# Kernel tuning notes

Hardware: AMD Instinct MI355X
Metric: run time of the kernel (lower is better)

Reference implementation:

```python
import jax, jax.numpy as jnp
import numpy as np

ALPHA = 0.05
KSIZE = 7
SIGMA = 7.0  # SecondMomentMatrixLayer calls get_gaussian_kernel(ksize, ksize)


def _gaussian_kernel(ksize, sigma):
    ax = np.arange(ksize, dtype=np.float32) - (ksize - 1) / 2.0
    g1 = np.exp(-(ax ** 2) / (2.0 * sigma ** 2))
    g2 = np.outer(g1, g1)
    g2 = g2 / g2.sum()
    return jnp.asarray(g2, dtype=jnp.float32)


def setup_inputs() -> dict:
    key = jax.random.key(0)
    x = jax.random.uniform(key, (1, 1, 2048, 4096), dtype=jnp.float32)
    # Sobel filters (cross-correlation weights, as torch conv2d uses)
    wx = jnp.array([[-1., 0., 1.], [-2., 0., 2.], [-1., 0., 1.]], dtype=jnp.float32)
    wy = wx.T
    sobel_w = jnp.stack([wx, wy], axis=0)[:, None]  # (2,1,3,3)
    gauss_w = _gaussian_kernel(KSIZE, SIGMA)[None, None]  # (1,1,7,7)
    return {"x": x, "sobel_w": sobel_w, "gauss_w": gauss_w}


def _conv_same(x, w, groups=1):
    # x: (N,C,H,W), w: (O,C/g,kh,kw); torch-style cross-correlation, SAME padding
    return jax.lax.conv_general_dilated(
        x, w, window_strides=(1, 1), padding="SAME",
        dimension_numbers=("NCHW", "OIHW", "NCHW"),
        feature_group_count=groups)


def reference(x, sobel_w, gauss_w):
    # 1) image gradients: (N,1,H,W) -> (N,2,H,W)
    g = _conv_same(x, sobel_w)
    ix, iy = g[:, 0], g[:, 1]  # (N,H,W)
    # 2) channel products Ixx, Iyy, Ixy: (N,3,H,W)
    prod = jnp.stack([ix * ix, iy * iy, ix * iy], axis=1)
    # 3) Gaussian smoothing of each channel (same kernel depthwise)
    gw3 = jnp.broadcast_to(gauss_w, (3, 1, KSIZE, KSIZE))
    s = _conv_same(prod, gw3, groups=3)
    sxx, syy, sxy = s[:, 0], s[:, 1], s[:, 2]  # (N,H,W)
    # 4) corner response R = det - alpha*trace^2 (with the original's extra unsqueeze(0))
    r = (sxx * syy - sxy * sxy) - ALPHA * ((sxx + syy) ** 2)[None]  # (1,N,H,W) -> (1,1,H,W) for N=1
    # 5) NMS: threshold at (lower) median, 7x7 stride-1 maxpool, equality mask, multiply
    flat = r.ravel()
    k = (flat.shape[0] - 1) // 2  # torch.median -> lower median
    med = jnp.partition(flat, k)[k]
    thr = jnp.where(r > med, r, jnp.float32(0))
    pooled = jax.lax.reduce_window(
        thr, -jnp.inf, jax.lax.max, (1, 1, KSIZE, KSIZE), (1, 1, 1, 1), "SAME")
    mask = jnp.where(pooled == thr, jnp.float32(1), jnp.float32(0))
    return mask * r
```

## Files before the change

### kernel.cpp

```cpp
#include <hip/hip_runtime.h>
#include <hip/hip_bf16.h>
#include <math.h>

#define H 2048
#define W 4096
#define NPIX (H * W)
#define KSEL 4194303u
#define NT 512
#define TSX 64
#define TSY 32
#define NBX (W / TSX)
#define NBY (H / TSY)

__device__ __forceinline__ unsigned fmap(float f) {
    unsigned u = __float_as_uint(f);
    return (u & 0x80000000u) ? ~u : (u | 0x80000000u);
}
__device__ __forceinline__ float4 ld4s(const float* p) { return *(const float4*)p; }
__device__ __forceinline__ void st4s(float* p, float4 v) { *(float4*)p = v; }

#define SMF 13480
#define SXA(r,c) smem[5472 + (r)*76 + (c)]
#define GXA(r,c) smem[(r)*72 + (c)]
#define GYA(r,c) smem[2736 + (r)*72 + (c)]
#define H0A(r,c) smem[5472 + (r)*68 + (c)]
#define H1A(r,c) smem[8056 + (r)*68 + (c)]
#define H2A(r,c) smem[10640 + (r)*68 + (c)]

__global__ __launch_bounds__(NT) void k_response(const float* __restrict__ x,
                                                 const float* __restrict__ gw,
                                                 float* __restrict__ r,
                                                 unsigned* __restrict__ hist1) {
    __shared__ float smem[SMF];
    unsigned* lh = (unsigned*)&smem[13224];

    int tl = threadIdx.x;
    int bx = blockIdx.x & (NBX - 1);
    int by = blockIdx.x >> 6;
    int tx0 = bx * TSX, ty0 = by * TSY;

    float hwr[7], vwr[7];
    float g33 = gw[24];
#pragma unroll
    for (int b = 0; b < 7; ++b) hwr[b] = gw[21 + b];
#pragma unroll
    for (int a = 0; a < 7; ++a) vwr[a] = gw[a * 7 + 3] / g33;

    if (tl < 256) lh[tl] = 0;

#pragma unroll
    for (int it = 0; it < 2; ++it) {
        int task = tl + it * NT;
        if (task < 720) {
            int row = task / 18, g = task - row * 18;
            int gy = ty0 - 4 + row;
            int gx0 = tx0 - 4 + 4 * g;
            float4 v = make_float4(0.f, 0.f, 0.f, 0.f);
            if ((unsigned)gy < H) {
                if ((unsigned)gx0 <= (unsigned)(W - 4)) {
                    v = *(const float4*)&x[(size_t)gy * W + gx0];
                } else {
                    float* vv = (float*)&v;
#pragma unroll
                    for (int k = 0; k < 4; ++k) {
                        int c = gx0 + k;
                        if ((unsigned)c < W) vv[k] = x[(size_t)gy * W + c];
                    }
                }
            }
            st4s(&SXA(row, 4 * g), v);
        }
    }
    __syncthreads();

#pragma unroll
    for (int it = 0; it < 2; ++it) {
        int task = tl + it * NT;
        if (task < 684) {
            int row = task / 18, g = task - row * 18;
            int base = 4 * g;
            float w0[8], w1[8], w2[8];
            {
                float4 t0 = ld4s(&SXA(row, base)), t1 = ld4s(&SXA(row, base + 4));
                w0[0]=t0.x; w0[1]=t0.y; w0[2]=t0.z; w0[3]=t0.w; w0[4]=t1.x; w0[5]=t1.y; w0[6]=t1.z; w0[7]=t1.w;
                t0 = ld4s(&SXA(row + 1, base)); t1 = ld4s(&SXA(row + 1, base + 4));
                w1[0]=t0.x; w1[1]=t0.y; w1[2]=t0.z; w1[3]=t0.w; w1[4]=t1.x; w1[5]=t1.y; w1[6]=t1.z; w1[7]=t1.w;
                t0 = ld4s(&SXA(row + 2, base)); t1 = ld4s(&SXA(row + 2, base + 4));
                w2[0]=t0.x; w2[1]=t0.y; w2[2]=t0.z; w2[3]=t0.w; w2[4]=t1.x; w2[5]=t1.y; w2[6]=t1.z; w2[7]=t1.w;
            }
            int rowOK = ((unsigned)(ty0 - 3 + row) < H);
            float4 gxv, gyv;
            float* pgx = (float*)&gxv;
            float* pgy = (float*)&gyv;
#pragma unroll
            for (int k = 0; k < 4; ++k) {
                float ixv = (w0[k + 2] - w0[k]) + 2.f * (w1[k + 2] - w1[k]) + (w2[k + 2] - w2[k]);
                float iyv = (w2[k] - w0[k]) + 2.f * (w2[k + 1] - w0[k + 1]) + (w2[k + 2] - w0[k + 2]);
                int gc = tx0 + base + k - 3;
                bool ok = rowOK && ((unsigned)gc < W);
                pgx[k] = ok ? ixv : 0.f;
                pgy[k] = ok ? iyv : 0.f;
            }
            st4s(&GXA(row, base), gxv);
            st4s(&GYA(row, base), gyv);
        }
    }
    __syncthreads();

#pragma unroll
    for (int it = 0; it < 2; ++it) {
        int task = tl + it * NT;
        if (task < 608) {
            int row = task >> 4, c0 = (task & 15) * 4;
            float wgx[12], wgy[12];
            {
                float4 t0 = ld4s(&GXA(row, c0)), t1 = ld4s(&GXA(row, c0 + 4)), t2 = ld4s(&GXA(row, c0 + 8));
                wgx[0]=t0.x; wgx[1]=t0.y; wgx[2]=t0.z; wgx[3]=t0.w; wgx[4]=t1.x; wgx[5]=t1.y; wgx[6]=t1.z; wgx[7]=t1.w;
                wgx[8]=t2.x; wgx[9]=t2.y; wgx[10]=t2.z; wgx[11]=t2.w;
                t0 = ld4s(&GYA(row, c0)); t1 = ld4s(&GYA(row, c0 + 4)); t2 = ld4s(&GYA(row, c0 + 8));
                wgy[0]=t0.x; wgy[1]=t0.y; wgy[2]=t0.z; wgy[3]=t0.w; wgy[4]=t1.x; wgy[5]=t1.y; wgy[6]=t1.z; wgy[7]=t1.w;
                wgy[8]=t2.x; wgy[9]=t2.y; wgy[10]=t2.z; wgy[11]=t2.w;
            }
            float px[10], py[10], pxy[10];
#pragma unroll
            for (int i = 0; i < 10; ++i) {
                px[i] = wgx[i] * wgx[i];
                py[i] = wgy[i] * wgy[i];
                pxy[i] = wgx[i] * wgy[i];
            }
            float4 s0, s1, s2;
            float* q0 = (float*)&s0; float* q1 = (float*)&s1; float* q2 = (float*)&s2;
#pragma unroll
            for (int k = 0; k < 4; ++k) {
                float a0 = 0.f, a1 = 0.f, a2 = 0.f;
#pragma unroll
                for (int b = 0; b < 7; ++b) {
                    float w = hwr[b];
                    a0 += w * px[k + b];
                    a1 += w * py[k + b];
                    a2 += w * pxy[k + b];
                }
                q0[k] = a0; q1[k] = a1; q2[k] = a2;
            }
            st4s(&H0A(row, c0), s0);
            st4s(&H1A(row, c0), s1);
            st4s(&H2A(row, c0), s2);
        }
    }
    __syncthreads();

    {
        int ii = tl >> 4, c0 = (tl & 15) * 4;
        float4 a0 = make_float4(0.f, 0.f, 0.f, 0.f), a1 = a0, a2 = a0;
#pragma unroll
        for (int a = 0; a < 7; ++a) {
            float w = vwr[a];
            float4 h0v = ld4s(&H0A(ii + a, c0));
            float4 h1v = ld4s(&H1A(ii + a, c0));
            float4 h2v = ld4s(&H2A(ii + a, c0));
            a0.x += w * h0v.x; a0.y += w * h0v.y; a0.z += w * h0v.z; a0.w += w * h0v.w;
            a1.x += w * h1v.x; a1.y += w * h1v.y; a1.z += w * h1v.z; a1.w += w * h1v.w;
            a2.x += w * h2v.x; a2.y += w * h2v.y; a2.z += w * h2v.z; a2.w += w * h2v.w;
        }
        float* sxx = (float*)&a0; float* syy = (float*)&a1; float* sxy = (float*)&a2;
        float4 rv4;
        float* prv = (float*)&rv4;
#pragma unroll
        for (int k = 0; k < 4; ++k) {
            float tr = sxx[k] + syy[k];
            float rv = sxx[k] * syy[k] - sxy[k] * sxy[k] - 0.05f * tr * tr;
            prv[k] = rv;
        }
        st4s(&r[(size_t)(ty0 + ii) * W + tx0 + c0], rv4);
#pragma unroll
        for (int k = 0; k < 4; ++k) atomicAdd(&lh[fmap(prv[k]) >> 24], 1u);
    }
    __syncthreads();
    if (tl < 256 && lh[tl]) atomicAdd(&hist1[tl], lh[tl]);
}

__global__ __launch_bounds__(256) void k_scan256(const unsigned* __restrict__ hist,
                                                 unsigned* __restrict__ sel,
                                                 int in_rank_idx, int out_base) {
    __shared__ unsigned s[256];
    int t = threadIdx.x;
    unsigned c = hist[t];
    s[t] = c;
    __syncthreads();
    for (int off = 1; off < 256; off <<= 1) {
        unsigned v = (t >= off) ? s[t - off] : 0u;
        __syncthreads();
        s[t] += v;
        __syncthreads();
    }
    unsigned k = (in_rank_idx < 0) ? KSEL : sel[in_rank_idx];
    unsigned cumb = s[t] - c;
    if (k >= cumb && k < s[t]) {
        sel[out_base] = (unsigned)t;
        sel[out_base + 1] = k - cumb;
    }
}

__global__ __launch_bounds__(256) void k_hist2(const float* __restrict__ r,
                                               const unsigned* __restrict__ sel,
                                               unsigned* __restrict__ hist2) {
    __shared__ unsigned lh[256];
    lh[threadIdx.x] = 0;
    __syncthreads();
    unsigned b1 = sel[0];
    int idx = blockIdx.x * blockDim.x + threadIdx.x;
    int stride = gridDim.x * blockDim.x;
    const float4* r4 = (const float4*)r;
    for (int i = idx; i < NPIX / 4; i += stride) {
        float4 v = r4[i];
        unsigned u;
        u = fmap(v.x); if ((u >> 24) == b1) atomicAdd(&lh[(u >> 16) & 0xFF], 1u);
        u = fmap(v.y); if ((u >> 24) == b1) atomicAdd(&lh[(u >> 16) & 0xFF], 1u);
        u = fmap(v.z); if ((u >> 24) == b1) atomicAdd(&lh[(u >> 16) & 0xFF], 1u);
        u = fmap(v.w); if ((u >> 24) == b1) atomicAdd(&lh[(u >> 16) & 0xFF], 1u);
    }
    __syncthreads();
    if (lh[threadIdx.x]) atomicAdd(&hist2[threadIdx.x], lh[threadIdx.x]);
}

__global__ __launch_bounds__(256) void k_hist3(const float* __restrict__ r,
                                               const unsigned* __restrict__ sel,
                                               unsigned* __restrict__ hist3) {
    unsigned top16 = (sel[0] << 8) | sel[2];
    int idx = blockIdx.x * blockDim.x + threadIdx.x;
    int stride = gridDim.x * blockDim.x;
    const float4* r4 = (const float4*)r;
    for (int i = idx; i < NPIX / 4; i += stride) {
        float4 v = r4[i];
        unsigned u;
        u = fmap(v.x); if ((u >> 16) == top16) atomicAdd(&hist3[u & 0xFFFF], 1u);
        u = fmap(v.y); if ((u >> 16) == top16) atomicAdd(&hist3[u & 0xFFFF], 1u);
        u = fmap(v.z); if ((u >> 16) == top16) atomicAdd(&hist3[u & 0xFFFF], 1u);
        u = fmap(v.w); if ((u >> 16) == top16) atomicAdd(&hist3[u & 0xFFFF], 1u);
    }
}

__global__ __launch_bounds__(256) void k_scan64k(const unsigned* __restrict__ hist3,
                                                 unsigned* __restrict__ sel) {
    __shared__ unsigned s[256];
    int t = threadIdx.x;
    unsigned sum = 0;
    for (int i = 0; i < 256; ++i) sum += hist3[t * 256 + i];
    s[t] = sum;
    __syncthreads();
    for (int off = 1; off < 256; off <<= 1) {
        unsigned v = (t >= off) ? s[t - off] : 0u;
        __syncthreads();
        s[t] += v;
        __syncthreads();
    }
    unsigned k = sel[3];
    unsigned cumb = s[t] - sum;
    if (k >= cumb && k < s[t]) {
        unsigned rem = k - cumb;
        unsigned cum = 0, b3 = 0;
        for (int i = 0; i < 256; ++i) {
            unsigned c = hist3[t * 256 + i];
            if (rem < cum + c) { b3 = (unsigned)(t * 256 + i); break; }
            cum += c;
        }
        unsigned med_u = (sel[0] << 24) | (sel[2] << 16) | b3;
        unsigned bits = (med_u & 0x80000000u) ? (med_u & 0x7FFFFFFFu) : ~med_u;
        ((float*)sel)[4] = __uint_as_float(bits);
    }
}

#define RTA(r,c) smem[(r)*76 + (c)]
#define THA(r,c) smem[2888 + (r)*76 + (c)]
#define HMA(r,c) smem[5776 + (r)*68 + (c)]

__global__ __launch_bounds__(NT) void k_final(const float* __restrict__ r,
                                              const unsigned* __restrict__ sel,
                                              float* __restrict__ out) {
    __shared__ float smem[8360];
    float med = ((const float*)sel)[4];
    int tl = threadIdx.x;
    int bx = blockIdx.x & (NBX - 1);
    int by = blockIdx.x >> 6;
    int tx0 = bx * TSX, ty0 = by * TSY;
    const float NINF = -INFINITY;

#pragma unroll
    for (int it = 0; it < 2; ++it) {
        int task = tl + it * NT;
        if (task < 684) {
            int row = task / 18, g = task - row * 18;
            int gy = ty0 - 3 + row;
            int gx0 = tx0 - 4 + 4 * g;
            float4 v = make_float4(NINF, NINF, NINF, NINF);
            float4 tv = v;
            float* pv = (float*)&v; float* ptv = (float*)&tv;
            if ((unsigned)gy < H) {
                if ((unsigned)gx0 <= (unsigned)(W - 4)) {
                    v = *(const float4*)&r[(size_t)gy * W + gx0];
#pragma unroll
                    for (int k = 0; k < 4; ++k) ptv[k] = (pv[k] > med) ? pv[k] : 0.f;
                } else {
#pragma unroll
                    for (int k = 0; k < 4; ++k) {
                        int c = gx0 + k;
                        if ((unsigned)c < W) {
                            float rv = r[(size_t)gy * W + c];
                            pv[k] = rv;
                            ptv[k] = (rv > med) ? rv : 0.f;
                        }
                    }
                }
            }
            st4s(&RTA(row, 4 * g), v);
            st4s(&THA(row, 4 * g), tv);
        }
    }
    __syncthreads();

#pragma unroll
    for (int it = 0; it < 2; ++it) {
        int task = tl + it * NT;
        if (task < 608) {
            int row = task >> 4, c0 = (task & 15) * 4;
            float w[12];
            {
                float4 t0 = ld4s(&THA(row, c0)), t1 = ld4s(&THA(row, c0 + 4)), t2 = ld4s(&THA(row, c0 + 8));
                w[0]=t0.x; w[1]=t0.y; w[2]=t0.z; w[3]=t0.w; w[4]=t1.x; w[5]=t1.y; w[6]=t1.z; w[7]=t1.w;
                w[8]=t2.x; w[9]=t2.y; w[10]=t2.z; w[11]=t2.w;
            }
            float4 m4;
            float* pm = (float*)&m4;
#pragma unroll
            for (int k = 0; k < 4; ++k) {
                float m = w[k + 1];
#pragma unroll
                for (int b = 2; b < 8; ++b) m = fmaxf(m, w[k + b]);
                pm[k] = m;
            }
            st4s(&HMA(row, c0), m4);
        }
    }
    __syncthreads();

    {
        int ii = tl >> 4, c0 = (tl & 15) * 4;
        float4 m = ld4s(&HMA(ii, c0));
#pragma unroll
        for (int a = 1; a < 7; ++a) {
            float4 h = ld4s(&HMA(ii + a, c0));
            m.x = fmaxf(m.x, h.x); m.y = fmaxf(m.y, h.y);
            m.z = fmaxf(m.z, h.z); m.w = fmaxf(m.w, h.w);
        }
        float4 rv = ld4s(&RTA(ii + 3, c0 + 4));
        float4 tv = ld4s(&THA(ii + 3, c0 + 4));
        float4 o;
        o.x = (m.x == tv.x) ? rv.x : 0.f;
        o.y = (m.y == tv.y) ? rv.y : 0.f;
        o.z = (m.z == tv.z) ? rv.z : 0.f;
        o.w = (m.w == tv.w) ? rv.w : 0.f;
        st4s(&out[(size_t)(ty0 + ii) * W + tx0 + c0], o);
    }
}

extern "C" void kernel_launch(void* const* d_in, const int* in_sizes, int n_in,
                              void* d_out, int out_size, void* d_ws, size_t ws_size,
                              hipStream_t stream) {
    const float* x = (const float*)d_in[0];
    const float* gw = (const float*)d_in[2];
    float* out = (float*)d_out;

    char* ws = (char*)d_ws;
    float* r = (float*)ws;
    unsigned* hist1 = (unsigned*)(ws + (size_t)NPIX * 4);
    unsigned* hist2 = hist1 + 256;
    unsigned* hist3 = hist2 + 256;
    unsigned* sel = hist3 + 65536;

    hipMemsetAsync(hist1, 0, (256 + 256 + 65536 + 8) * sizeof(unsigned), stream);

    int nblk = NBX * NBY;
    k_response<<<nblk, NT, 0, stream>>>(x, gw, r, hist1);
    k_scan256<<<1, 256, 0, stream>>>(hist1, sel, -1, 0);
    k_hist2<<<1024, 256, 0, stream>>>(r, sel, hist2);
    k_scan256<<<1, 256, 0, stream>>>(hist2, sel, 1, 2);
    k_hist3<<<1024, 256, 0, stream>>>(r, sel, hist3);
    k_scan64k<<<1, 256, 0, stream>>>(hist3, sel);
    k_final<<<nblk, NT, 0, stream>>>(r, sel, out);
}
```

Measured before the change: 140.7 us.

## Add interior fast paths, widen 64k scan, drop threshold tile from NMS kernel

Interior tiles in the response and final kernels now skip boundary checks on halo loads and Sobel masking. The final-stage median scan runs with 1024 threads using vectorized uint4 loads, which shortens each thread's serial loop. The NMS kernel no longer stores a separate thresholded tile in shared memory; it recomputes the threshold in registers, which cuts shared-memory footprint and stores. The median slot moves from sel[4] to sel[6], which adds an extra branch for -inf padding.

```diff
diff --git a/kernel.cpp b/kernel.cpp
--- a/kernel.cpp
+++ b/kernel.cpp
@@ -18,6 +18,12 @@
 }
 __device__ __forceinline__ float4 ld4s(const float* p) { return *(const float4*)p; }
 __device__ __forceinline__ void st4s(float* p, float4 v) { *(float4*)p = v; }
+__device__ __forceinline__ void ld12(const float* p, float* d) {
+    float4 a = ld4s(p), b = ld4s(p + 4), c = ld4s(p + 8);
+    d[0]=a.x; d[1]=a.y; d[2]=a.z; d[3]=a.w;
+    d[4]=b.x; d[5]=b.y; d[6]=b.z; d[7]=b.w;
+    d[8]=c.x; d[9]=c.y; d[10]=c.z; d[11]=c.w;
+}
 
 #define SMF 13480
 #define SXA(r,c) smem[5472 + (r)*76 + (c)]
@@ -38,6 +44,7 @@
     int bx = blockIdx.x & (NBX - 1);
     int by = blockIdx.x >> 6;
     int tx0 = bx * TSX, ty0 = by * TSY;
+    bool interior = ((unsigned)(bx - 1) < 62u) && ((unsigned)(by - 1) < 62u);
 
     float hwr[7], vwr[7];
     float g33 = gw[24];
@@ -55,16 +62,21 @@
             int row = task / 18, g = task - row * 18;
             int gy = ty0 - 4 + row;
             int gx0 = tx0 - 4 + 4 * g;
-            float4 v = make_float4(0.f, 0.f, 0.f, 0.f);
-            if ((unsigned)gy < H) {
-                if ((unsigned)gx0 <= (unsigned)(W - 4)) {
-                    v = *(const float4*)&x[(size_t)gy * W + gx0];
-                } else {
-                    float* vv = (float*)&v;
-#pragma unroll
-                    for (int k = 0; k < 4; ++k) {
-                        int c = gx0 + k;
-                        if ((unsigned)c < W) vv[k] = x[(size_t)gy * W + c];
+            float4 v;
+            if (interior) {
+                v = *(const float4*)&x[(size_t)gy * W + gx0];
+            } else {
+                v = make_float4(0.f, 0.f, 0.f, 0.f);
+                if ((unsigned)gy < H) {
+                    if ((unsigned)gx0 <= (unsigned)(W - 4)) {
+                        v = *(const float4*)&x[(size_t)gy * W + gx0];
+                    } else {
+                        float* vv = (float*)&v;
+#pragma unroll
+                        for (int k = 0; k < 4; ++k) {
+                            int c = gx0 + k;
+                            if ((unsigned)c < W) vv[k] = x[(size_t)gy * W + c];
+                        }
                     }
                 }
             }
@@ -88,18 +100,26 @@
                 t0 = ld4s(&SXA(row + 2, base)); t1 = ld4s(&SXA(row + 2, base + 4));
                 w2[0]=t0.x; w2[1]=t0.y; w2[2]=t0.z; w2[3]=t0.w; w2[4]=t1.x; w2[5]=t1.y; w2[6]=t1.z; w2[7]=t1.w;
             }
-            int rowOK = ((unsigned)(ty0 - 3 + row) < H);
             float4 gxv, gyv;
             float* pgx = (float*)&gxv;
             float* pgy = (float*)&gyv;
-#pragma unroll
-            for (int k = 0; k < 4; ++k) {
-                float ixv = (w0[k + 2] - w0[k]) + 2.f * (w1[k + 2] - w1[k]) + (w2[k + 2] - w2[k]);
-                float iyv = (w2[k] - w0[k]) + 2.f * (w2[k + 1] - w0[k + 1]) + (w2[k + 2] - w0[k + 2]);
-                int gc = tx0 + base + k - 3;
-                bool ok = rowOK && ((unsigned)gc < W);
-                pgx[k] = ok ? ixv : 0.f;
-                pgy[k] = ok ? iyv : 0.f;
+            if (interior) {
+#pragma unroll
+                for (int k = 0; k < 4; ++k) {
+                    pgx[k] = (w0[k + 2] - w0[k]) + 2.f * (w1[k + 2] - w1[k]) + (w2[k + 2] - w2[k]);
+                    pgy[k] = (w2[k] - w0[k]) + 2.f * (w2[k + 1] - w0[k + 1]) + (w2[k + 2] - w0[k + 2]);
+                }
+            } else {
+                int rowOK = ((unsigned)(ty0 - 3 + row) < H);
+#pragma unroll
+                for (int k = 0; k < 4; ++k) {
+                    float ixv = (w0[k + 2] - w0[k]) + 2.f * (w1[k + 2] - w1[k]) + (w2[k + 2] - w2[k]);
+                    float iyv = (w2[k] - w0[k]) + 2.f * (w2[k + 1] - w0[k + 1]) + (w2[k + 2] - w0[k + 2]);
+                    int gc = tx0 + base + k - 3;
+                    bool ok = rowOK && ((unsigned)gc < W);
+                    pgx[k] = ok ? ixv : 0.f;
+                    pgy[k] = ok ? iyv : 0.f;
+                }
             }
             st4s(&GXA(row, base), gxv);
             st4s(&GYA(row, base), gyv);
@@ -113,14 +133,8 @@
         if (task < 608) {
             int row = task >> 4, c0 = (task & 15) * 4;
             float wgx[12], wgy[12];
-            {
-                float4 t0 = ld4s(&GXA(row, c0)), t1 = ld4s(&GXA(row, c0 + 4)), t2 = ld4s(&GXA(row, c0 + 8));
-                wgx[0]=t0.x; wgx[1]=t0.y; wgx[2]=t0.z; wgx[3]=t0.w; wgx[4]=t1.x; wgx[5]=t1.y; wgx[6]=t1.z; wgx[7]=t1.w;
-                wgx[8]=t2.x; wgx[9]=t2.y; wgx[10]=t2.z; wgx[11]=t2.w;
-                t0 = ld4s(&GYA(row, c0)); t1 = ld4s(&GYA(row, c0 + 4)); t2 = ld4s(&GYA(row, c0 + 8));
-                wgy[0]=t0.x; wgy[1]=t0.y; wgy[2]=t0.z; wgy[3]=t0.w; wgy[4]=t1.x; wgy[5]=t1.y; wgy[6]=t1.z; wgy[7]=t1.w;
-                wgy[8]=t2.x; wgy[9]=t2.y; wgy[10]=t2.z; wgy[11]=t2.w;
-            }
+            ld12(&GXA(row, c0), wgx);
+            ld12(&GYA(row, c0), wgy);
             float px[10], py[10], pxy[10];
 #pragma unroll
             for (int i = 0; i < 10; ++i) {
@@ -168,8 +182,7 @@
 #pragma unroll
         for (int k = 0; k < 4; ++k) {
             float tr = sxx[k] + syy[k];
-            float rv = sxx[k] * syy[k] - sxy[k] * sxy[k] - 0.05f * tr * tr;
-            prv[k] = rv;
+            prv[k] = sxx[k] * syy[k] - sxy[k] * sxy[k] - 0.05f * tr * tr;
         }
         st4s(&r[(size_t)(ty0 + ii) * W + tx0 + c0], rv4);
 #pragma unroll
@@ -240,49 +253,54 @@
     }
 }
 
-__global__ __launch_bounds__(256) void k_scan64k(const unsigned* __restrict__ hist3,
-                                                 unsigned* __restrict__ sel) {
-    __shared__ unsigned s[256];
+__global__ __launch_bounds__(1024) void k_scan64k(const unsigned* __restrict__ hist3,
+                                                  unsigned* __restrict__ sel) {
+    __shared__ unsigned ps[1024];
     int t = threadIdx.x;
+    const uint4* h4 = (const uint4*)hist3;
     unsigned sum = 0;
-    for (int i = 0; i < 256; ++i) sum += hist3[t * 256 + i];
-    s[t] = sum;
-    __syncthreads();
-    for (int off = 1; off < 256; off <<= 1) {
-        unsigned v = (t >= off) ? s[t - off] : 0u;
+#pragma unroll
+    for (int i = 0; i < 16; ++i) {
+        uint4 v = h4[t * 16 + i];
+        sum += v.x + v.y + v.z + v.w;
+    }
+    ps[t] = sum;
+    __syncthreads();
+    for (int off = 1; off < 1024; off <<= 1) {
+        unsigned v = (t >= off) ? ps[t - off] : 0u;
         __syncthreads();
-        s[t] += v;
+        ps[t] += v;
         __syncthreads();
     }
     unsigned k = sel[3];
-    unsigned cumb = s[t] - sum;
-    if (k >= cumb && k < s[t]) {
+    unsigned inc = ps[t], cumb = inc - sum;
+    if (k >= cumb && k < inc) {
         unsigned rem = k - cumb;
         unsigned cum = 0, b3 = 0;
-        for (int i = 0; i < 256; ++i) {
-            unsigned c = hist3[t * 256 + i];
-            if (rem < cum + c) { b3 = (unsigned)(t * 256 + i); break; }
+        for (int i = 0; i < 64; ++i) {
+            unsigned c = hist3[t * 64 + i];
+            if (rem < cum + c) { b3 = (unsigned)(t * 64 + i); break; }
             cum += c;
         }
         unsigned med_u = (sel[0] << 24) | (sel[2] << 16) | b3;
         unsigned bits = (med_u & 0x80000000u) ? (med_u & 0x7FFFFFFFu) : ~med_u;
-        ((float*)sel)[4] = __uint_as_float(bits);
-    }
-}
-
-#define RTA(r,c) smem[(r)*76 + (c)]
-#define THA(r,c) smem[2888 + (r)*76 + (c)]
-#define HMA(r,c) smem[5776 + (r)*68 + (c)]
+        ((float*)sel)[6] = __uint_as_float(bits);
+    }
+}
+
+#define RT(r,c) smem[(r)*72 + (c)]
+#define HM(r,c) smem[2736 + (r)*64 + (c)]
 
 __global__ __launch_bounds__(NT) void k_final(const float* __restrict__ r,
                                               const unsigned* __restrict__ sel,
                                               float* __restrict__ out) {
-    __shared__ float smem[8360];
-    float med = ((const float*)sel)[4];
+    __shared__ float smem[5168];
+    float med = ((const float*)sel)[6];
     int tl = threadIdx.x;
     int bx = blockIdx.x & (NBX - 1);
     int by = blockIdx.x >> 6;
     int tx0 = bx * TSX, ty0 = by * TSY;
+    bool interior = ((unsigned)(bx - 1) < 62u) && ((unsigned)(by - 1) < 62u);
     const float NINF = -INFINITY;
 
 #pragma unroll
@@ -292,28 +310,25 @@
             int row = task / 18, g = task - row * 18;
             int gy = ty0 - 3 + row;
             int gx0 = tx0 - 4 + 4 * g;
-            float4 v = make_float4(NINF, NINF, NINF, NINF);
-            float4 tv = v;
-            float* pv = (float*)&v; float* ptv = (float*)&tv;
-            if ((unsigned)gy < H) {
-                if ((unsigned)gx0 <= (unsigned)(W - 4)) {
-                    v = *(const float4*)&r[(size_t)gy * W + gx0];
-#pragma unroll
-                    for (int k = 0; k < 4; ++k) ptv[k] = (pv[k] > med) ? pv[k] : 0.f;
-                } else {
-#pragma unroll
-                    for (int k = 0; k < 4; ++k) {
-                        int c = gx0 + k;
-                        if ((unsigned)c < W) {
-                            float rv = r[(size_t)gy * W + c];
-                            pv[k] = rv;
-                            ptv[k] = (rv > med) ? rv : 0.f;
+            float4 v;
+            if (interior) {
+                v = *(const float4*)&r[(size_t)gy * W + gx0];
+            } else {
+                v = make_float4(NINF, NINF, NINF, NINF);
+                if ((unsigned)gy < H) {
+                    if ((unsigned)gx0 <= (unsigned)(W - 4)) {
+                        v = *(const float4*)&r[(size_t)gy * W + gx0];
+                    } else {
+                        float* pv = (float*)&v;
+#pragma unroll
+                        for (int k = 0; k < 4; ++k) {
+                            int c = gx0 + k;
+                            if ((unsigned)c < W) pv[k] = r[(size_t)gy * W + c];
                         }
                     }
                 }
             }
-            st4s(&RTA(row, 4 * g), v);
-            st4s(&THA(row, 4 * g), tv);
+            st4s(&RT(row, 4 * g), v);
         }
     }
     __syncthreads();
@@ -322,43 +337,48 @@
     for (int it = 0; it < 2; ++it) {
         int task = tl + it * NT;
         if (task < 608) {
-            int row = task >> 4, c0 = (task & 15) * 4;
+            int row = task >> 4, c0 = (task & 15) << 2;
             float w[12];
-            {
-                float4 t0 = ld4s(&THA(row, c0)), t1 = ld4s(&THA(row, c0 + 4)), t2 = ld4s(&THA(row, c0 + 8));
-                w[0]=t0.x; w[1]=t0.y; w[2]=t0.z; w[3]=t0.w; w[4]=t1.x; w[5]=t1.y; w[6]=t1.z; w[7]=t1.w;
-                w[8]=t2.x; w[9]=t2.y; w[10]=t2.z; w[11]=t2.w;
+            ld12(&RT(row, c0), w);
+            float th[11];
+#pragma unroll
+            for (int j = 1; j <= 10; ++j) {
+                float v = w[j];
+                th[j] = (v > med) ? v : ((v == NINF) ? NINF : 0.f);
             }
             float4 m4;
             float* pm = (float*)&m4;
 #pragma unroll
             for (int k = 0; k < 4; ++k) {
-                float m = w[k + 1];
-#pragma unroll
-                for (int b = 2; b < 8; ++b) m = fmaxf(m, w[k + b]);
+                float m = th[k + 1];
+#pragma unroll
+                for (int b = 2; b < 8; ++b) m = fmaxf(m, th[k + b]);
                 pm[k] = m;
             }
-            st4s(&HMA(row, c0), m4);
+            st4s(&HM(row, c0), m4);
         }
     }
     __syncthreads();
 
     {
-        int ii = tl >> 4, c0 = (tl & 15) * 4;
-        float4 m = ld4s(&HMA(ii, c0));
+        int ii = tl >> 4, c0 = (tl & 15) << 2;
+        float4 m = ld4s(&HM(ii, c0));
 #pragma unroll
         for (int a = 1; a < 7; ++a) {
-            float4 h = ld4s(&HMA(ii + a, c0));
+            float4 h = ld4s(&HM(ii + a, c0));
             m.x = fmaxf(m.x, h.x); m.y = fmaxf(m.y, h.y);
             m.z = fmaxf(m.z, h.z); m.w = fmaxf(m.w, h.w);
         }
-        float4 rv = ld4s(&RTA(ii + 3, c0 + 4));
-        float4 tv = ld4s(&THA(ii + 3, c0 + 4));
+        float4 rv = ld4s(&RT(ii + 3, c0 + 4));
         float4 o;
-        o.x = (m.x == tv.x) ? rv.x : 0.f;
-        o.y = (m.y == tv.y) ? rv.y : 0.f;
-        o.z = (m.z == tv.z) ? rv.z : 0.f;
-        o.w = (m.w == tv.w) ? rv.w : 0.f;
+        float tvx = (rv.x > med) ? rv.x : 0.f;
+        float tvy = (rv.y > med) ? rv.y : 0.f;
+        float tvz = (rv.z > med) ? rv.z : 0.f;
+        float tvw = (rv.w > med) ? rv.w : 0.f;
+        o.x = (m.x == tvx) ? rv.x : 0.f;
+        o.y = (m.y == tvy) ? rv.y : 0.f;
+        o.z = (m.z == tvz) ? rv.z : 0.f;
+        o.w = (m.w == tvw) ? rv.w : 0.f;
         st4s(&out[(size_t)(ty0 + ii) * W + tx0 + c0], o);
     }
 }
@@ -385,6 +405,6 @@
     k_hist2<<<1024, 256, 0, stream>>>(r, sel, hist2);
     k_scan256<<<1, 256, 0, stream>>>(hist2, sel, 1, 2);
     k_hist3<<<1024, 256, 0, stream>>>(r, sel, hist3);
-    k_scan64k<<<1, 256, 0, stream>>>(hist3, sel);
+    k_scan64k<<<1, 1024, 0, stream>>>(hist3, sel);
     k_final<<<nblk, NT, 0, stream>>>(r, sel, out);
 }
```

Result: no change. 142.6 us (+1.3%).
